# Optimization experiments

Measured on AMD Instinct MI355X. Metric: run time of the kernel, lower is better.

The kernel has to match this reference:

```python
import jax, jax.numpy as jnp
import numpy as np

N = 50000      # nodes
E = 800000     # edges (avg degree 16)
C = 256        # channels
NOUT = 64      # n_out (hidden width of last conv's MLP)
NL = 4         # n_layers


def _glorot(key, shape):
    fan_in, fan_out = shape[-2], shape[-1]
    lim = np.sqrt(6.0 / (fan_in + fan_out)).astype(np.float32)
    return jax.random.uniform(key, shape, jnp.float32, -lim, lim)


def setup_inputs() -> dict:
    key = jax.random.key(0)
    ks = jax.random.split(key, 16)
    inp = {
        "x": jax.random.normal(ks[0], (N, C), jnp.float32),
        "src": jax.random.randint(ks[1], (E,), 0, N, jnp.int32),
        "dst": jax.random.randint(ks[2], (E,), 0, N, jnp.int32),
        # 3 inner GINConv MLPs: Dense(C,relu), Dense(C,relu), Dense(C,linear)
        "W1s": _glorot(ks[3], (NL - 1, C, C)),
        "b1s": jax.random.normal(ks[4], (NL - 1, C), jnp.float32) * 0.01,
        "W2s": _glorot(ks[5], (NL - 1, C, C)),
        "b2s": jax.random.normal(ks[6], (NL - 1, C), jnp.float32) * 0.01,
        "W3s": _glorot(ks[7], (NL - 1, C, C)),
        "b3s": jax.random.normal(ks[8], (NL - 1, C), jnp.float32) * 0.01,
        # final conv2 MLP: Dense(C,relu), Dense(NOUT,relu), Dense(C,linear)
        "cW1": _glorot(ks[9], (C, C)),
        "cb1": jax.random.normal(ks[10], (C,), jnp.float32) * 0.01,
        "cW2": _glorot(ks[11], (C, NOUT)),
        "cb2": jax.random.normal(ks[12], (NOUT,), jnp.float32) * 0.01,
        "cW3": _glorot(ks[13], (NOUT, C)),
        "cb3": jax.random.normal(ks[14], (C,), jnp.float32) * 0.01,
    }
    return inp


def reference(x, src, dst, W1s, b1s, W2s, b2s, W3s, b3s,
              cW1, cb1, cW2, cb2, cW3, cb3):
    def agg(h):
        # sparse A @ h: sum messages from src nodes into dst nodes
        return jax.ops.segment_sum(h[src], dst, num_segments=N)

    # inner GINConv layers (eps=0 -> (1+eps)*x == x)
    for l in range(NL - 1):
        h = x + agg(x)                       # [N, C]
        h = jax.nn.relu(h @ W1s[l] + b1s[l])
        h = jax.nn.relu(h @ W2s[l] + b2s[l])
        x = h @ W3s[l] + b3s[l]              # final Dense is linear

    # conv2: mlp_hidden=[C, NOUT] (relu) then final Dense(C, linear)
    h = x + agg(x)
    h = jax.nn.relu(h @ cW1 + cb1)
    h = jax.nn.relu(h @ cW2 + cb2)
    return h @ cW3 + cb3                     # [N, C]
```

## Files before the change

### kernel.cpp

```cpp
#include <hip/hip_runtime.h>

constexpr int C_DIM = 256;

using f32x4  = __attribute__((ext_vector_type(4))) float;
using bf16x8 = __attribute__((ext_vector_type(8))) short;

__device__ __forceinline__ float uf(uint u) { return __uint_as_float(u); }
__device__ __forceinline__ uint  fu(float f) { return __float_as_uint(f); }

typedef __attribute__((address_space(3))) unsigned int lds_u32;
typedef const __attribute__((address_space(1))) unsigned int glb_u32;

__device__ __forceinline__ void gll16(const ushort* g, ushort* l) {
    __builtin_amdgcn_global_load_lds((glb_u32*)g, (lds_u32*)l, 16, 0, 0);
}


__global__ void k_zero_i32(int* __restrict__ p, int n) {
    int i = blockIdx.x * blockDim.x + threadIdx.x;
    if (i < n) p[i] = 0;
}

__global__ void k_hist(const int* __restrict__ dst, int E, int* __restrict__ cnt) {
    int e = blockIdx.x * blockDim.x + threadIdx.x;
    if (e < E) atomicAdd(&cnt[dst[e]], 1);
}

__global__ __launch_bounds__(1024) void k_scan(const int* __restrict__ cnt,
                                               int* __restrict__ off, int n) {
    __shared__ int sh[1024];
    const int tid = threadIdx.x;
    const int chunk = (n + 1023) >> 10;
    const int s = tid * chunk;
    const int e = min(s + chunk, n);
    int sum = 0;
    for (int i = s; i < e; i++) sum += cnt[i];
    sh[tid] = sum;
    __syncthreads();
    for (int ofs = 1; ofs < 1024; ofs <<= 1) {
        int t = (tid >= ofs) ? sh[tid - ofs] : 0;
        __syncthreads();
        sh[tid] += t;
        __syncthreads();
    }
    int run = sh[tid] - sum;
    for (int i = s; i < e; i++) { off[i] = run; run += cnt[i]; }
    if (tid == 1023) off[n] = sh[1023];
}

__global__ void k_copy_i32(const int* __restrict__ a, int* __restrict__ b, int n) {
    int i = blockIdx.x * blockDim.x + threadIdx.x;
    if (i < n) b[i] = a[i];
}

__global__ void k_scatter(const int* __restrict__ src, const int* __restrict__ dst, int E,
                          int* __restrict__ cur, int* __restrict__ adj) {
    int e = blockIdx.x * blockDim.x + threadIdx.x;
    if (e < E) {
        int p = atomicAdd(&cur[dst[e]], 1);
        adj[p] = src[e];
    }
}

template <int SPLIT_IN>
__global__ __launch_bounds__(256) void k_agg2(const float* __restrict__ xf,
        const ushort* __restrict__ xh, const ushort* __restrict__ xl,
        const int* __restrict__ off, const int* __restrict__ adj,
        ushort* __restrict__ Hh, ushort* __restrict__ Hl, int n) {
    const int node = blockIdx.x * 4 + (threadIdx.x >> 6);
    if (node >= n) return;
    const int lane = threadIdx.x & 63;
    float a0, a1, a2, a3;
    if (SPLIT_IN) {
        const uint2 h  = ((const uint2*)(xh + (size_t)node * C_DIM))[lane];
        const uint2 lo = ((const uint2*)(xl + (size_t)node * C_DIM))[lane];
        a0 = uf(h.x << 16) + uf(lo.x << 16);
        a1 = uf(h.x & 0xffff0000u) + uf(lo.x & 0xffff0000u);
        a2 = uf(h.y << 16) + uf(lo.y << 16);
        a3 = uf(h.y & 0xffff0000u) + uf(lo.y & 0xffff0000u);
    } else {
        const float4 v = ((const float4*)(xf + (size_t)node * C_DIM))[lane];
        a0 = v.x; a1 = v.y; a2 = v.z; a3 = v.w;
    }
    const int s = off[node], e = off[node + 1];
    for (int j = s; j < e; j++) {
        const int sn = adj[j];
        if (SPLIT_IN) {
            const uint2 h  = ((const uint2*)(xh + (size_t)sn * C_DIM))[lane];
            const uint2 lo = ((const uint2*)(xl + (size_t)sn * C_DIM))[lane];
            a0 += uf(h.x << 16) + uf(lo.x << 16);
            a1 += uf(h.x & 0xffff0000u) + uf(lo.x & 0xffff0000u);
            a2 += uf(h.y << 16) + uf(lo.y << 16);
            a3 += uf(h.y & 0xffff0000u) + uf(lo.y & 0xffff0000u);
        } else {
            const float4 v = ((const float4*)(xf + (size_t)sn * C_DIM))[lane];
            a0 += v.x; a1 += v.y; a2 += v.z; a3 += v.w;
        }
    }
    const uint u0 = fu(a0), u1 = fu(a1), u2 = fu(a2), u3 = fu(a3);
    uint2 ho, lo_;
    ho.x = (u0 >> 16) | (u1 & 0xffff0000u);
    ho.y = (u2 >> 16) | (u3 & 0xffff0000u);
    const float r0 = a0 - uf(u0 & 0xffff0000u);
    const float r1 = a1 - uf(u1 & 0xffff0000u);
    const float r2 = a2 - uf(u2 & 0xffff0000u);
    const float r3 = a3 - uf(u3 & 0xffff0000u);
    lo_.x = (fu(r0) >> 16) | (fu(r1) & 0xffff0000u);
    lo_.y = (fu(r2) >> 16) | (fu(r3) & 0xffff0000u);
    ((uint2*)(Hh + (size_t)node * C_DIM))[lane] = ho;
    ((uint2*)(Hl + (size_t)node * C_DIM))[lane] = lo_;
}

__global__ void k_split_w(const float* __restrict__ W, ushort* __restrict__ hi,
                          ushort* __restrict__ lo, int K, int M, int total) {
    int i = blockIdx.x * blockDim.x + threadIdx.x;
    if (i >= total) return;
    const int KM = K * M;
    const int mi = i / KM, rem = i - mi * KM;
    const int k = rem / M, m = rem - k * M;
    const float x = W[i];
    const uint u = fu(x);
    const float lf = x - uf(u & 0xffff0000u);
    const int oidx = mi * KM + m * K + k;
    hi[oidx] = (ushort)(u >> 16);
    lo[oidx] = (ushort)(fu(lf) >> 16);
}

template <int RELU, int OSPLIT>
__global__ __launch_bounds__(256) void k_gemm5(const ushort* __restrict__ Ah,
        const ushort* __restrict__ Al, const ushort* __restrict__ Bh,
        const ushort* __restrict__ Bl, const float* __restrict__ bias,
        float* __restrict__ Yf, ushort* __restrict__ Yh, ushort* __restrict__ Yl,
        int n, int K, int M) {
    __shared__ ushort AsH[128 * 32], AsL[128 * 32], BsH[64 * 32], BsL[64 * 32];
    const int tid = threadIdx.x;
    const int l = tid & 63, w = tid >> 6;
    const int wr = w >> 1, wc = w & 1;
    const int lr = l & 15, lkq = l >> 4;
    const int row0 = blockIdx.x * 128, col0 = blockIdx.y * 64;
    f32x4 acc[4][2] = {};

    const int lsub = l >> 2;
    const int lkb  = (((l & 3) ^ ((l >> 3) & 3)) * 8);
    const int swz  = (lkq ^ ((lr >> 1) & 3)) * 8;

    for (int k0 = 0; k0 < K; k0 += 32) {
        __syncthreads();
        for (int c = w; c < 24; c += 4) {
            if (c < 16) {
                const int a = c & 7;
                const int grow = min(row0 + a * 16 + lsub, n - 1);
                const ushort* gp = (c < 8 ? Ah : Al) + (size_t)grow * K + k0 + lkb;
                ushort* lp = (c < 8 ? AsH : AsL) + a * 512;
                gll16(gp, lp);
            } else {
                const int a = c & 3;
                const int col = col0 + a * 16 + lsub;
                const ushort* gp = (c < 20 ? Bh : Bl) + (size_t)col * K + k0 + lkb;
                ushort* lp = (c < 20 ? BsH : BsL) + a * 512;
                gll16(gp, lp);
            }
        }
        __syncthreads();

        bf16x8 aH[4], aL[4], bH[2], bL[2];
#pragma unroll
        for (int f = 0; f < 4; f++) {
            const int r = (wr * 64 + f * 16 + lr) * 32 + swz;
            aH[f] = *(const bf16x8*)&AsH[r];
            aL[f] = *(const bf16x8*)&AsL[r];
        }
#pragma unroll
        for (int f = 0; f < 2; f++) {
            const int r = (wc * 32 + f * 16 + lr) * 32 + swz;
            bH[f] = *(const bf16x8*)&BsH[r];
            bL[f] = *(const bf16x8*)&BsL[r];
        }
#pragma unroll
        for (int fi = 0; fi < 4; fi++)
#pragma unroll
            for (int fj = 0; fj < 2; fj++) {
                acc[fi][fj] = __builtin_amdgcn_mfma_f32_16x16x32_bf16(aH[fi], bH[fj], acc[fi][fj], 0, 0, 0);
                acc[fi][fj] = __builtin_amdgcn_mfma_f32_16x16x32_bf16(aL[fi], bH[fj], acc[fi][fj], 0, 0, 0);
                acc[fi][fj] = __builtin_amdgcn_mfma_f32_16x16x32_bf16(aH[fi], bL[fj], acc[fi][fj], 0, 0, 0);
            }
    }

#pragma unroll
    for (int fi = 0; fi < 4; fi++)
#pragma unroll
        for (int fj = 0; fj < 2; fj++) {
            const int col = col0 + wc * 32 + fj * 16 + lr;
            const float bv = bias[col];
#pragma unroll
            for (int r = 0; r < 4; r++) {
                const int row = row0 + wr * 64 + fi * 16 + lkq * 4 + r;
                if (row < n) {
                    float v = acc[fi][fj][r] + bv;
                    if (RELU) v = fmaxf(v, 0.f);
                    const size_t oi = (size_t)row * M + col;
                    if (OSPLIT) {
                        const uint u = fu(v);
                        const float rv = v - uf(u & 0xffff0000u);
                        Yh[oi] = (ushort)(u >> 16);
                        Yl[oi] = (ushort)(fu(rv) >> 16);
                    } else {
                        Yf[oi] = v;
                    }
                }
            }
        }
}


extern "C" void kernel_launch(void* const* d_in, const int* in_sizes, int n_in,
                              void* d_out, int out_size, void* d_ws, size_t ws_size,
                              hipStream_t stream) {
    const float* x   = (const float*)d_in[0];
    const int*   src = (const int*)d_in[1];
    const int*   dst = (const int*)d_in[2];
    const float* W1s = (const float*)d_in[3];
    const float* b1s = (const float*)d_in[4];
    const float* W2s = (const float*)d_in[5];
    const float* b2s = (const float*)d_in[6];
    const float* W3s = (const float*)d_in[7];
    const float* b3s = (const float*)d_in[8];
    const float* cW1 = (const float*)d_in[9];
    const float* cb1 = (const float*)d_in[10];
    const float* cW2 = (const float*)d_in[11];
    const float* cb2 = (const float*)d_in[12];
    const float* cW3 = (const float*)d_in[13];
    const float* cb3 = (const float*)d_in[14];

    const int n  = in_sizes[0] / C_DIM;
    const int E  = in_sizes[1];
    const int NL = in_sizes[3] / (C_DIM * C_DIM);

    char* wsp = (char*)d_ws;
    size_t o = 0;
    auto take = [&](size_t bytes) -> char* {
        char* p = wsp + o;
        o = (o + bytes + 255) & ~(size_t)255;
        return p;
    };
    int* off = (int*)take(sizeof(int) * (size_t)(n + 1));
    int* cur = (int*)take(sizeof(int) * (size_t)n);
    int* adj = (int*)take(sizeof(int) * (size_t)E);
    const size_t plane = (size_t)n * C_DIM;
    ushort* B0h = (ushort*)take(2 * plane);
    ushort* B0l = (ushort*)take(2 * plane);
    ushort* B1h = (ushort*)take(2 * plane);
    ushort* B1l = (ushort*)take(2 * plane);
    ushort* B2h = (ushort*)d_out;
    ushort* B2l = B2h + plane;

    const int szW  = NL * C_DIM * C_DIM;
    const int szC1 = C_DIM * C_DIM;
    const int szC2 = C_DIM * 64;
    const int szC3 = 64 * C_DIM;
    ushort* W1tH = (ushort*)take(2ull * szW);
    ushort* W1tL = (ushort*)take(2ull * szW);
    ushort* W2tH = (ushort*)take(2ull * szW);
    ushort* W2tL = (ushort*)take(2ull * szW);
    ushort* W3tH = (ushort*)take(2ull * szW);
    ushort* W3tL = (ushort*)take(2ull * szW);
    ushort* C1tH = (ushort*)take(2ull * szC1);
    ushort* C1tL = (ushort*)take(2ull * szC1);
    ushort* C2tH = (ushort*)take(2ull * szC2);
    ushort* C2tL = (ushort*)take(2ull * szC2);
    ushort* C3tH = (ushort*)take(2ull * szC3);
    ushort* C3tL = (ushort*)take(2ull * szC3);
    float* out = (float*)d_out;

    const dim3 b256(256);

    k_split_w<<<dim3((szW + 255) / 256), b256, 0, stream>>>(W1s, W1tH, W1tL, C_DIM, C_DIM, szW);
    k_split_w<<<dim3((szW + 255) / 256), b256, 0, stream>>>(W2s, W2tH, W2tL, C_DIM, C_DIM, szW);
    k_split_w<<<dim3((szW + 255) / 256), b256, 0, stream>>>(W3s, W3tH, W3tL, C_DIM, C_DIM, szW);
    k_split_w<<<dim3((szC1 + 255) / 256), b256, 0, stream>>>(cW1, C1tH, C1tL, C_DIM, C_DIM, szC1);
    k_split_w<<<dim3((szC2 + 255) / 256), b256, 0, stream>>>(cW2, C2tH, C2tL, C_DIM, 64, szC2);
    k_split_w<<<dim3((szC3 + 255) / 256), b256, 0, stream>>>(cW3, C3tH, C3tL, 64, C_DIM, szC3);

    k_zero_i32<<<dim3((n + 255) / 256), b256, 0, stream>>>(cur, n);
    k_hist<<<dim3((E + 255) / 256), b256, 0, stream>>>(dst, E, cur);
    k_scan<<<1, 1024, 0, stream>>>(cur, off, n);
    k_copy_i32<<<dim3((n + 255) / 256), b256, 0, stream>>>(off, cur, n);
    k_scatter<<<dim3((E + 255) / 256), b256, 0, stream>>>(src, dst, E, cur, adj);

    const int gx = (n + 127) / 128;
    const dim3 gAgg((n + 3) / 4);

    for (int lyr = 0; lyr < NL; lyr++) {
        const size_t wo = (size_t)lyr * C_DIM * C_DIM;
        if (lyr == 0)
            k_agg2<0><<<gAgg, b256, 0, stream>>>(x, nullptr, nullptr, off, adj, B1h, B1l, n);
        else
            k_agg2<1><<<gAgg, b256, 0, stream>>>(nullptr, B0h, B0l, off, adj, B1h, B1l, n);
        k_gemm5<1, 1><<<dim3(gx, 4), b256, 0, stream>>>(B1h, B1l, W1tH + wo, W1tL + wo,
            b1s + lyr * C_DIM, nullptr, B2h, B2l, n, C_DIM, C_DIM);
        k_gemm5<1, 1><<<dim3(gx, 4), b256, 0, stream>>>(B2h, B2l, W2tH + wo, W2tL + wo,
            b2s + lyr * C_DIM, nullptr, B1h, B1l, n, C_DIM, C_DIM);
        k_gemm5<0, 1><<<dim3(gx, 4), b256, 0, stream>>>(B1h, B1l, W3tH + wo, W3tL + wo,
            b3s + lyr * C_DIM, nullptr, B0h, B0l, n, C_DIM, C_DIM);
    }

    k_agg2<1><<<gAgg, b256, 0, stream>>>(nullptr, B0h, B0l, off, adj, B1h, B1l, n);
    k_gemm5<1, 1><<<dim3(gx, 4), b256, 0, stream>>>(B1h, B1l, C1tH, C1tL, cb1,
        nullptr, B2h, B2l, n, C_DIM, C_DIM);
    k_gemm5<1, 1><<<dim3(gx, 1), b256, 0, stream>>>(B2h, B2l, C2tH, C2tL, cb2,
        nullptr, B1h, B1l, n, C_DIM, 64);
    k_gemm5<0, 0><<<dim3(gx, 4), b256, 0, stream>>>(B1h, B1l, C3tH, C3tL, cb3,
        out, nullptr, nullptr, n, 64, C_DIM);
}
```

Baseline: 1.433 ms.

## Use full-width column tiles in split-bf16 GEMM to read activations once

Reshapes the GEMM block tile from 128x64 with a 4-way column grid to 64 rows by the full output width (BN templated as 256 or 64). Each block now loads its activation rows once and computes every output column, removing the 4x redundant reads of the hi/lo activation arrays. The trade-off is larger LDS use for weights, more weight loads per block, lower B-fragment reuse per MFMA, and fewer, larger blocks.

```diff
diff --git a/kernel.cpp b/kernel.cpp
--- a/kernel.cpp
+++ b/kernel.cpp
@@ -126,19 +126,23 @@
     lo[oidx] = (ushort)(fu(lf) >> 16);
 }
 
-template <int RELU, int OSPLIT>
-__global__ __launch_bounds__(256) void k_gemm5(const ushort* __restrict__ Ah,
+template <int RELU, int OSPLIT, int BN>
+__global__ __launch_bounds__(256) void k_gemm7(const ushort* __restrict__ Ah,
         const ushort* __restrict__ Al, const ushort* __restrict__ Bh,
         const ushort* __restrict__ Bl, const float* __restrict__ bias,
         float* __restrict__ Yf, ushort* __restrict__ Yh, ushort* __restrict__ Yl,
-        int n, int K, int M) {
-    __shared__ ushort AsH[128 * 32], AsL[128 * 32], BsH[64 * 32], BsL[64 * 32];
+        int n, int K) {
+    constexpr int NBC = BN / 16;
+    constexpr int NCHUNK = 8 + 2 * NBC;
+    constexpr int NF = BN / 32;
+    __shared__ ushort AsH[64 * 32], AsL[64 * 32], BsH[BN * 32], BsL[BN * 32];
+
     const int tid = threadIdx.x;
     const int l = tid & 63, w = tid >> 6;
     const int wr = w >> 1, wc = w & 1;
     const int lr = l & 15, lkq = l >> 4;
-    const int row0 = blockIdx.x * 128, col0 = blockIdx.y * 64;
-    f32x4 acc[4][2] = {};
+    const int row0 = blockIdx.x * 64;
+    f32x4 acc[2][NF] = {};
 
     const int lsub = l >> 2;
     const int lkb  = (((l & 3) ^ ((l >> 3) & 3)) * 8);
@@ -146,59 +150,58 @@
 
     for (int k0 = 0; k0 < K; k0 += 32) {
         __syncthreads();
-        for (int c = w; c < 24; c += 4) {
-            if (c < 16) {
-                const int a = c & 7;
+        for (int c = w; c < NCHUNK; c += 4) {
+            if (c < 8) {
+                const int a = c & 3;
                 const int grow = min(row0 + a * 16 + lsub, n - 1);
-                const ushort* gp = (c < 8 ? Ah : Al) + (size_t)grow * K + k0 + lkb;
-                ushort* lp = (c < 8 ? AsH : AsL) + a * 512;
+                const ushort* gp = (c < 4 ? Ah : Al) + (size_t)grow * K + k0 + lkb;
+                ushort* lp = (c < 4 ? AsH : AsL) + a * 512;
                 gll16(gp, lp);
             } else {
-                const int a = c & 3;
-                const int col = col0 + a * 16 + lsub;
-                const ushort* gp = (c < 20 ? Bh : Bl) + (size_t)col * K + k0 + lkb;
-                ushort* lp = (c < 20 ? BsH : BsL) + a * 512;
+                const int bc = c - 8;
+                const int cc = bc & (NBC - 1);
+                const int col = cc * 16 + lsub;
+                const ushort* gp = (bc < NBC ? Bh : Bl) + (size_t)col * K + k0 + lkb;
+                ushort* lp = (bc < NBC ? BsH : BsL) + cc * 512;
                 gll16(gp, lp);
             }
         }
         __syncthreads();
 
-        bf16x8 aH[4], aL[4], bH[2], bL[2];
-#pragma unroll
-        for (int f = 0; f < 4; f++) {
-            const int r = (wr * 64 + f * 16 + lr) * 32 + swz;
-            aH[f] = *(const bf16x8*)&AsH[r];
-            aL[f] = *(const bf16x8*)&AsL[r];
-        }
-#pragma unroll
-        for (int f = 0; f < 2; f++) {
-            const int r = (wc * 32 + f * 16 + lr) * 32 + swz;
-            bH[f] = *(const bf16x8*)&BsH[r];
-            bL[f] = *(const bf16x8*)&BsL[r];
-        }
-#pragma unroll
-        for (int fi = 0; fi < 4; fi++)
-#pragma unroll
-            for (int fj = 0; fj < 2; fj++) {
-                acc[fi][fj] = __builtin_amdgcn_mfma_f32_16x16x32_bf16(aH[fi], bH[fj], acc[fi][fj], 0, 0, 0);
-                acc[fi][fj] = __builtin_amdgcn_mfma_f32_16x16x32_bf16(aL[fi], bH[fj], acc[fi][fj], 0, 0, 0);
-                acc[fi][fj] = __builtin_amdgcn_mfma_f32_16x16x32_bf16(aH[fi], bL[fj], acc[fi][fj], 0, 0, 0);
+        bf16x8 aH[2], aL[2];
+#pragma unroll
+        for (int fi = 0; fi < 2; fi++) {
+            const int rr = (wr * 32 + fi * 16 + lr) * 32 + swz;
+            aH[fi] = *(const bf16x8*)&AsH[rr];
+            aL[fi] = *(const bf16x8*)&AsL[rr];
+        }
+#pragma unroll
+        for (int fj = 0; fj < NF; fj++) {
+            const int rr = (wc * (BN / 2) + fj * 16 + lr) * 32 + swz;
+            const bf16x8 bH = *(const bf16x8*)&BsH[rr];
+            const bf16x8 bL = *(const bf16x8*)&BsL[rr];
+#pragma unroll
+            for (int fi = 0; fi < 2; fi++) {
+                acc[fi][fj] = __builtin_amdgcn_mfma_f32_16x16x32_bf16(aH[fi], bH, acc[fi][fj], 0, 0, 0);
+                acc[fi][fj] = __builtin_amdgcn_mfma_f32_16x16x32_bf16(aL[fi], bH, acc[fi][fj], 0, 0, 0);
+                acc[fi][fj] = __builtin_amdgcn_mfma_f32_16x16x32_bf16(aH[fi], bL, acc[fi][fj], 0, 0, 0);
             }
-    }
-
-#pragma unroll
-    for (int fi = 0; fi < 4; fi++)
-#pragma unroll
-        for (int fj = 0; fj < 2; fj++) {
-            const int col = col0 + wc * 32 + fj * 16 + lr;
+        }
+    }
+
+#pragma unroll
+    for (int fi = 0; fi < 2; fi++)
+#pragma unroll
+        for (int fj = 0; fj < NF; fj++) {
+            const int col = wc * (BN / 2) + fj * 16 + lr;
             const float bv = bias[col];
 #pragma unroll
-            for (int r = 0; r < 4; r++) {
-                const int row = row0 + wr * 64 + fi * 16 + lkq * 4 + r;
+            for (int rg = 0; rg < 4; rg++) {
+                const int row = row0 + wr * 32 + fi * 16 + lkq * 4 + rg;
                 if (row < n) {
-                    float v = acc[fi][fj][r] + bv;
+                    float v = acc[fi][fj][rg] + bv;
                     if (RELU) v = fmaxf(v, 0.f);
-                    const size_t oi = (size_t)row * M + col;
+                    const size_t oi = (size_t)row * BN + col;
                     if (OSPLIT) {
                         const uint u = fu(v);
                         const float rv = v - uf(u & 0xffff0000u);
@@ -287,7 +290,7 @@
     k_copy_i32<<<dim3((n + 255) / 256), b256, 0, stream>>>(off, cur, n);
     k_scatter<<<dim3((E + 255) / 256), b256, 0, stream>>>(src, dst, E, cur, adj);
 
-    const int gx = (n + 127) / 128;
+    const int gx = (n + 63) / 64;
     const dim3 gAgg((n + 3) / 4);
 
     for (int lyr = 0; lyr < NL; lyr++) {
@@ -296,19 +299,19 @@
             k_agg2<0><<<gAgg, b256, 0, stream>>>(x, nullptr, nullptr, off, adj, B1h, B1l, n);
         else
             k_agg2<1><<<gAgg, b256, 0, stream>>>(nullptr, B0h, B0l, off, adj, B1h, B1l, n);
-        k_gemm5<1, 1><<<dim3(gx, 4), b256, 0, stream>>>(B1h, B1l, W1tH + wo, W1tL + wo,
-            b1s + lyr * C_DIM, nullptr, B2h, B2l, n, C_DIM, C_DIM);
-        k_gemm5<1, 1><<<dim3(gx, 4), b256, 0, stream>>>(B2h, B2l, W2tH + wo, W2tL + wo,
-            b2s + lyr * C_DIM, nullptr, B1h, B1l, n, C_DIM, C_DIM);
-        k_gemm5<0, 1><<<dim3(gx, 4), b256, 0, stream>>>(B1h, B1l, W3tH + wo, W3tL + wo,
-            b3s + lyr * C_DIM, nullptr, B0h, B0l, n, C_DIM, C_DIM);
+        k_gemm7<1, 1, 256><<<dim3(gx), b256, 0, stream>>>(B1h, B1l, W1tH + wo, W1tL + wo,
+            b1s + lyr * C_DIM, nullptr, B2h, B2l, n, C_DIM);
+        k_gemm7<1, 1, 256><<<dim3(gx), b256, 0, stream>>>(B2h, B2l, W2tH + wo, W2tL + wo,
+            b2s + lyr * C_DIM, nullptr, B1h, B1l, n, C_DIM);
+        k_gemm7<0, 1, 256><<<dim3(gx), b256, 0, stream>>>(B1h, B1l, W3tH + wo, W3tL + wo,
+            b3s + lyr * C_DIM, nullptr, B0h, B0l, n, C_DIM);
     }
 
     k_agg2<1><<<gAgg, b256, 0, stream>>>(nullptr, B0h, B0l, off, adj, B1h, B1l, n);
-    k_gemm5<1, 1><<<dim3(gx, 4), b256, 0, stream>>>(B1h, B1l, C1tH, C1tL, cb1,
-        nullptr, B2h, B2l, n, C_DIM, C_DIM);
-    k_gemm5<1, 1><<<dim3(gx, 1), b256, 0, stream>>>(B2h, B2l, C2tH, C2tL, cb2,
-        nullptr, B1h, B1l, n, C_DIM, 64);
-    k_gemm5<0, 0><<<dim3(gx, 4), b256, 0, stream>>>(B1h, B1l, C3tH, C3tL, cb3,
-        out, nullptr, nullptr, n, 64, C_DIM);
-}
+    k_gemm7<1, 1, 256><<<dim3(gx), b256, 0, stream>>>(B1h, B1l, C1tH, C1tL, cb1,
+        nullptr, B2h, B2l, n, C_DIM);
+    k_gemm7<1, 1, 64><<<dim3(gx), b256, 0, stream>>>(B2h, B2l, C2tH, C2tL, cb2,
+        nullptr, B1h, B1l, n, C_DIM);
+    k_gemm7<0, 0, 256><<<dim3(gx), b256, 0, stream>>>(B1h, B1l, C3tH, C3tL, cb3,
+        out, nullptr, nullptr, n, 64);
+}
```

After: 1.332 ms. 7.1% less time.
